# Kernel tuning notes

Measured on AMD Instinct MI355X. Metric: run time of the kernel, lower is better.

## Reference

```python
import jax, jax.numpy as jnp
import numpy as np

EMBED_DIM = 64
N_POINTS = 1_000_000


def sinusoidal_embedding(vals, embed_dim):
    # vals: [B] float -> [B, embed_dim]
    half = embed_dim // 2
    log_scale = np.log(10000.0) / (half - 1)
    freqs = jnp.exp(jnp.arange(half, dtype=jnp.float32) * (-log_scale))
    ang = vals[:, None] * freqs[None, :]
    return jnp.concatenate([jnp.sin(ang), jnp.cos(ang)], axis=1)


def embed_mlp(x, w1, b1, w2, b2):
    # Linear -> LeakyReLU(0.1) -> Linear  (embedf / embedm)
    h = jax.nn.leaky_relu(x @ w1.T + b1, negative_slope=0.1)
    return h @ w2.T + b2


def setup_inputs() -> dict:
    key = jax.random.key(0)
    ks = jax.random.split(key, 12)
    d, dh = EMBED_DIM, EMBED_DIM // 2
    s = lambda fan_in: 1.0 / np.sqrt(fan_in)
    return {
        "inputs": jax.random.normal(ks[0], (1, 6, N_POINTS), dtype=jnp.float32),
        "t": jax.random.uniform(ks[1], (1,), dtype=jnp.float32) * 1000.0,
        "mask": jax.random.randint(ks[2], (N_POINTS,), 0, 2, dtype=jnp.int32),
        "pdf": jax.random.normal(ks[3], (N_POINTS, d), dtype=jnp.float32),
        # embedf params: Linear(d,d), Linear(d,d//2)
        "ef_w1": jax.random.uniform(ks[4], (d, d), minval=-s(d), maxval=s(d)),
        "ef_b1": jnp.zeros((d,), jnp.float32),
        "ef_w2": jax.random.uniform(ks[5], (dh, d), minval=-s(d), maxval=s(d)),
        "ef_b2": jnp.zeros((dh,), jnp.float32),
        # embedm params
        "em_w1": jax.random.uniform(ks[6], (d, d), minval=-s(d), maxval=s(d)),
        "em_b1": jnp.zeros((d,), jnp.float32),
        "em_w2": jax.random.uniform(ks[7], (dh, d), minval=-s(d), maxval=s(d)),
        "em_b2": jnp.zeros((dh,), jnp.float32),
    }


def reference(inputs, t, mask, pdf, ef_w1, ef_b1, ef_w2, ef_b2, em_w1, em_b1, em_w2, em_b2):
    n = inputs.shape[-1]
    # pdf branch: [N, 64] -> [1, 64, N]
    pdf_cnl = pdf.T[None]  # [1, 64, N]
    # timestep embedding -> embedf -> broadcast over points
    te = embed_mlp(sinusoidal_embedding(t, EMBED_DIM), ef_w1, ef_b1, ef_w2, ef_b2)  # [1, 32]
    temb = jnp.broadcast_to(te[:, :, None], (te.shape[0], te.shape[1], n))  # [1, 32, N]
    # per-point mask embedding -> embedm
    me = embed_mlp(sinusoidal_embedding(mask.astype(jnp.float32), EMBED_DIM), em_w1, em_b1, em_w2, em_b2)  # [N, 32]
    memb = me.T[None]  # [1, 32, N]
    temb = jnp.concatenate([temb, memb], axis=1)  # [1, 64, N]
    # return conditioning tensors produced by the (truncated) forward prefix
    return jnp.concatenate([pdf_cnl, temb], axis=1)  # [1, 128, N]
```

## Files before the change

### kernel.cpp

```cpp
#include <hip/hip_runtime.h>
#include <math.h>


#define HALF 32

typedef float v4f __attribute__((ext_vector_type(4)));

__global__ void embed_small_kernel(const float* __restrict__ t,
                                   const float* __restrict__ ef_w1, const float* __restrict__ ef_b1,
                                   const float* __restrict__ ef_w2, const float* __restrict__ ef_b2,
                                   const float* __restrict__ em_w1, const float* __restrict__ em_b1,
                                   const float* __restrict__ em_w2, const float* __restrict__ em_b2,
                                   float* __restrict__ ws) {
    __shared__ float h[3][64];
    const int tid = threadIdx.x;
    const float log_scale = 0.2970934777f;

    if (tid < 192) {
        const int v = tid >> 6;
        const int j = tid & 63;
        const float val = (v == 0) ? t[0] : (float)(v - 1);
        const float* w1 = (v == 0) ? ef_w1 : em_w1;
        const float* b1 = (v == 0) ? ef_b1 : em_b1;
        float acc = b1[j];
        for (int k = 0; k < HALF; ++k) {
            float f = expf(-(float)k * log_scale);
            float ang = val * f;
            float s, c;
            sincosf(ang, &s, &c);
            acc += s * w1[j * 64 + k] + c * w1[j * 64 + HALF + k];
        }
        h[v][j] = (acc > 0.0f) ? acc : 0.1f * acc;
    }
    __syncthreads();
    if (tid < 96) {
        const int v = tid >> 5;
        const int c = tid & 31;
        const float* w2 = (v == 0) ? ef_w2 : em_w2;
        const float* b2 = (v == 0) ? ef_b2 : em_b2;
        float acc = b2[c];
        for (int j = 0; j < 64; ++j) acc += h[v][j] * w2[c * 64 + j];
        ws[v * 32 + c] = acc;
    }
}

__global__ __launch_bounds__(256) void pvcnn_cond_kernel(
        const float* __restrict__ pdf,
        const int* __restrict__ mask,
        const float* __restrict__ ws,
        float* __restrict__ out,
        int N) {
    __shared__ float tile[64][65];
    __shared__ float emb[96];

    const int tid = threadIdx.x;

    const int nwg  = gridDim.x;
    const int q    = nwg >> 3;
    const int r    = nwg & 7;
    const int xcd  = blockIdx.x & 7;
    const int j    = blockIdx.x >> 3;
    const int bid  = (xcd < r ? xcd * (q + 1) : r * (q + 1) + (xcd - r) * q) + j;

    const long long p0 = (long long)bid * 64;
    const bool full = (p0 + 64 <= (long long)N);

    if (tid < 96) emb[tid] = ws[tid];

    if (full) {
        const v4f* pdf4 = (const v4f*)(pdf + p0 * 64);
        #pragma unroll
        for (int it = 0; it < 4; ++it) {
            int f = tid + it * 256;
            int p = f >> 4;
            int qq = f & 15;
            v4f v = pdf4[p * 16 + qq];
            tile[p][4 * qq + 0] = v.x;
            tile[p][4 * qq + 1] = v.y;
            tile[p][4 * qq + 2] = v.z;
            tile[p][4 * qq + 3] = v.w;
        }
    } else {
        #pragma unroll
        for (int it = 0; it < 4; ++it) {
            int f = tid + it * 256;
            int p = f >> 4;
            int qq = f & 15;
            v4f v = {0.f, 0.f, 0.f, 0.f};
            if (p0 + p < (long long)N) {
                const v4f* pdf4 = (const v4f*)(pdf + (p0 + p) * 64);
                v = pdf4[qq];
            }
            tile[p][4 * qq + 0] = v.x;
            tile[p][4 * qq + 1] = v.y;
            tile[p][4 * qq + 2] = v.z;
            tile[p][4 * qq + 3] = v.w;
        }
    }

    const int p  = tid & 63;
    const int wv = tid >> 6;
    const bool pok = (p0 + p < (long long)N);
    int mval = 0;
    if (pok) mval = mask[p0 + p];

    __syncthreads();

    if (pok) {
        const long long col = p0 + p;
        #pragma unroll
        for (int cb = 0; cb < 64; cb += 4) {
            int c = cb + wv;
            __builtin_nontemporal_store(tile[p][c], out + (long long)c * N + col);
        }
        #pragma unroll
        for (int cb = 0; cb < 32; cb += 4) {
            int c = cb + wv;
            __builtin_nontemporal_store(emb[c], out + (long long)(64 + c) * N + col);
        }
        #pragma unroll
        for (int cb = 0; cb < 32; cb += 4) {
            int c = cb + wv;
            __builtin_nontemporal_store(mval ? emb[64 + c] : emb[32 + c],
                                        out + (long long)(96 + c) * N + col);
        }
    }
}

extern "C" void kernel_launch(void* const* d_in, const int* in_sizes, int n_in,
                              void* d_out, int out_size, void* d_ws, size_t ws_size,
                              hipStream_t stream) {
    const float* t     = (const float*)d_in[1];
    const int*   mask  = (const int*)d_in[2];
    const float* pdf   = (const float*)d_in[3];
    const float* ef_w1 = (const float*)d_in[4];
    const float* ef_b1 = (const float*)d_in[5];
    const float* ef_w2 = (const float*)d_in[6];
    const float* ef_b2 = (const float*)d_in[7];
    const float* em_w1 = (const float*)d_in[8];
    const float* em_b1 = (const float*)d_in[9];
    const float* em_w2 = (const float*)d_in[10];
    const float* em_b2 = (const float*)d_in[11];

    float* out = (float*)d_out;
    float* ws  = (float*)d_ws;
    const int N = in_sizes[2];

    embed_small_kernel<<<1, 192, 0, stream>>>(t, ef_w1, ef_b1, ef_w2, ef_b2,
                                              em_w1, em_b1, em_w2, em_b2, ws);

    const int nblocks = (N + 63) / 64;
    pvcnn_cond_kernel<<<nblocks, 256, 0, stream>>>(pdf, mask, ws, out, N);
}
```

Before: 136.5 us.

## Split broadcast/mask rows into separate vectorized kernel from pdf transpose

Splits the fused kernel in two. One kernel writes the 64 embedding rows with 128-bit nontemporal stores, handling 4 columns per thread and loading the mask as int4. The other kernel only does the pdf transpose. The aim is to replace scalar 32-bit stores on the broadcast half of the output with wide stores, at the cost of an extra kernel launch and the loss of overlap between the two kinds of traffic.

```diff
diff --git a/kernel.cpp b/kernel.cpp
--- a/kernel.cpp
+++ b/kernel.cpp
@@ -5,6 +5,7 @@
 #define HALF 32
 
 typedef float v4f __attribute__((ext_vector_type(4)));
+typedef int   v4i __attribute__((ext_vector_type(4)));
 
 __global__ void embed_small_kernel(const float* __restrict__ t,
                                    const float* __restrict__ ef_w1, const float* __restrict__ ef_b1,
@@ -44,28 +45,90 @@
     }
 }
 
-__global__ __launch_bounds__(256) void pvcnn_cond_kernel(
-        const float* __restrict__ pdf,
+#define BC 1024
+
+__global__ __launch_bounds__(256) void bcast_kernel(
         const int* __restrict__ mask,
         const float* __restrict__ ws,
         float* __restrict__ out,
         int N) {
+    __shared__ float emb[96];
+    const int tid = threadIdx.x;
+
+    const int nwg = gridDim.x;
+    const int q   = nwg >> 3;
+    const int r8  = nwg & 7;
+    const int xcd = blockIdx.x & 7;
+    const int j8  = blockIdx.x >> 3;
+    const int bid = (xcd < r8 ? xcd * (q + 1) : r8 * (q + 1) + (xcd - r8) * q) + j8;
+
+    const long long c0 = (long long)bid * BC;
+    const bool full = (c0 + BC <= (long long)N);
+    const long long col = c0 + 4 * tid;
+
+    if (tid < 96) emb[tid] = ws[tid];
+
+    v4i m4 = {0, 0, 0, 0};
+    if (full) {
+        m4 = ((const v4i*)mask)[(c0 >> 2) + tid];
+    } else {
+        if (col + 0 < N) m4.x = mask[col + 0];
+        if (col + 1 < N) m4.y = mask[col + 1];
+        if (col + 2 < N) m4.z = mask[col + 2];
+        if (col + 3 < N) m4.w = mask[col + 3];
+    }
+    __syncthreads();
+
+    if (full) {
+        #pragma unroll
+        for (int c = 0; c < 32; ++c) {
+            const float e = emb[c];
+            const v4f v = (v4f){e, e, e, e};
+            __builtin_nontemporal_store(v, (v4f*)(out + (long long)(64 + c) * N + col));
+        }
+        #pragma unroll
+        for (int c = 0; c < 32; ++c) {
+            const float e0 = emb[32 + c];
+            const float e1 = emb[64 + c];
+            const v4f v = (v4f){m4.x ? e1 : e0, m4.y ? e1 : e0,
+                                m4.z ? e1 : e0, m4.w ? e1 : e0};
+            __builtin_nontemporal_store(v, (v4f*)(out + (long long)(96 + c) * N + col));
+        }
+    } else {
+        for (int c = 0; c < 32; ++c) {
+            const float e = emb[c];
+            for (int d = 0; d < 4; ++d)
+                if (col + d < (long long)N)
+                    out[(long long)(64 + c) * N + col + d] = e;
+        }
+        for (int c = 0; c < 32; ++c) {
+            const float e0 = emb[32 + c];
+            const float e1 = emb[64 + c];
+            const int mm[4] = {m4.x, m4.y, m4.z, m4.w};
+            for (int d = 0; d < 4; ++d)
+                if (col + d < (long long)N)
+                    out[(long long)(96 + c) * N + col + d] = mm[d] ? e1 : e0;
+        }
+    }
+}
+
+__global__ __launch_bounds__(256) void transpose_kernel(
+        const float* __restrict__ pdf,
+        float* __restrict__ out,
+        int N) {
     __shared__ float tile[64][65];
-    __shared__ float emb[96];
 
     const int tid = threadIdx.x;
 
-    const int nwg  = gridDim.x;
-    const int q    = nwg >> 3;
-    const int r    = nwg & 7;
-    const int xcd  = blockIdx.x & 7;
-    const int j    = blockIdx.x >> 3;
-    const int bid  = (xcd < r ? xcd * (q + 1) : r * (q + 1) + (xcd - r) * q) + j;
+    const int nwg = gridDim.x;
+    const int q   = nwg >> 3;
+    const int r8  = nwg & 7;
+    const int xcd = blockIdx.x & 7;
+    const int j8  = blockIdx.x >> 3;
+    const int bid = (xcd < r8 ? xcd * (q + 1) : r8 * (q + 1) + (xcd - r8) * q) + j8;
 
     const long long p0 = (long long)bid * 64;
     const bool full = (p0 + 64 <= (long long)N);
-
-    if (tid < 96) emb[tid] = ws[tid];
 
     if (full) {
         const v4f* pdf4 = (const v4f*)(pdf + p0 * 64);
@@ -101,8 +164,6 @@
     const int p  = tid & 63;
     const int wv = tid >> 6;
     const bool pok = (p0 + p < (long long)N);
-    int mval = 0;
-    if (pok) mval = mask[p0 + p];
 
     __syncthreads();
 
@@ -112,17 +173,6 @@
         for (int cb = 0; cb < 64; cb += 4) {
             int c = cb + wv;
             __builtin_nontemporal_store(tile[p][c], out + (long long)c * N + col);
-        }
-        #pragma unroll
-        for (int cb = 0; cb < 32; cb += 4) {
-            int c = cb + wv;
-            __builtin_nontemporal_store(emb[c], out + (long long)(64 + c) * N + col);
-        }
-        #pragma unroll
-        for (int cb = 0; cb < 32; cb += 4) {
-            int c = cb + wv;
-            __builtin_nontemporal_store(mval ? emb[64 + c] : emb[32 + c],
-                                        out + (long long)(96 + c) * N + col);
         }
     }
 }
@@ -149,6 +199,9 @@
     embed_small_kernel<<<1, 192, 0, stream>>>(t, ef_w1, ef_b1, ef_w2, ef_b2,
                                               em_w1, em_b1, em_w2, em_b2, ws);
 
-    const int nblocks = (N + 63) / 64;
-    pvcnn_cond_kernel<<<nblocks, 256, 0, stream>>>(pdf, mask, ws, out, N);
-}
+    const int nb_b = (N + BC - 1) / BC;
+    bcast_kernel<<<nb_b, 256, 0, stream>>>(mask, ws, out, N);
+
+    const int nb_t = (N + 63) / 64;
+    transpose_kernel<<<nb_t, 256, 0, stream>>>(pdf, out, N);
+}
```

After: 143.8 us. +5.4%, slower.

## Widen transpose tile to 256 points per 1024-thread block with column-major LDS

Applied to the files above, without the earlier changes.

Each block now handles 256 points with 1024 threads instead of 64 points with 256 threads. The shared tile is stored channel-major with padding, so each output row write covers 256 contiguous floats (1 KB) per block instead of 256 bytes. This is meant to improve write coalescing and cut block-scheduling overhead on a memory-bound transpose. In exchange, LDS use per block grows to about 66 KB, which lowers how many blocks fit on a CU, and the transposing LDS writes may hit more bank conflicts.

```diff
diff --git a/kernel.cpp b/kernel.cpp
--- a/kernel.cpp
+++ b/kernel.cpp
@@ -3,6 +3,7 @@
 
 
 #define HALF 32
+#define PTS 256
 
 typedef float v4f __attribute__((ext_vector_type(4)));
 
@@ -44,85 +45,96 @@
     }
 }
 
-__global__ __launch_bounds__(256) void pvcnn_cond_kernel(
+__global__ __launch_bounds__(1024) void pvcnn_cond_kernel(
         const float* __restrict__ pdf,
         const int* __restrict__ mask,
         const float* __restrict__ ws,
         float* __restrict__ out,
         int N) {
-    __shared__ float tile[64][65];
+    __shared__ float tile[64 * 257];
     __shared__ float emb[96];
 
     const int tid = threadIdx.x;
 
-    const int nwg  = gridDim.x;
-    const int q    = nwg >> 3;
-    const int r    = nwg & 7;
-    const int xcd  = blockIdx.x & 7;
-    const int j    = blockIdx.x >> 3;
-    const int bid  = (xcd < r ? xcd * (q + 1) : r * (q + 1) + (xcd - r) * q) + j;
+    const int nwg = gridDim.x;
+    const int q   = nwg >> 3;
+    const int r8  = nwg & 7;
+    const int xcd = blockIdx.x & 7;
+    const int j8  = blockIdx.x >> 3;
+    const int bid = (xcd < r8 ? xcd * (q + 1) : r8 * (q + 1) + (xcd - r8) * q) + j8;
 
-    const long long p0 = (long long)bid * 64;
-    const bool full = (p0 + 64 <= (long long)N);
+    const long long p0 = (long long)bid * PTS;
+    const bool full = (p0 + PTS <= (long long)N);
 
     if (tid < 96) emb[tid] = ws[tid];
 
     if (full) {
-        const v4f* pdf4 = (const v4f*)(pdf + p0 * 64);
+        const v4f* src = (const v4f*)(pdf + p0 * 64);
         #pragma unroll
         for (int it = 0; it < 4; ++it) {
-            int f = tid + it * 256;
-            int p = f >> 4;
-            int qq = f & 15;
-            v4f v = pdf4[p * 16 + qq];
-            tile[p][4 * qq + 0] = v.x;
-            tile[p][4 * qq + 1] = v.y;
-            tile[p][4 * qq + 2] = v.z;
-            tile[p][4 * qq + 3] = v.w;
+            const int f = tid + it * 1024;
+            const int p = f >> 4;
+            const int qq = f & 15;
+            const v4f v = src[f];
+            const int b = (4 * qq) * 257 + p;
+            tile[b + 0 * 257] = v.x;
+            tile[b + 1 * 257] = v.y;
+            tile[b + 2 * 257] = v.z;
+            tile[b + 3 * 257] = v.w;
         }
     } else {
         #pragma unroll
         for (int it = 0; it < 4; ++it) {
-            int f = tid + it * 256;
-            int p = f >> 4;
-            int qq = f & 15;
+            const int f = tid + it * 1024;
+            const int p = f >> 4;
+            const int qq = f & 15;
             v4f v = {0.f, 0.f, 0.f, 0.f};
-            if (p0 + p < (long long)N) {
-                const v4f* pdf4 = (const v4f*)(pdf + (p0 + p) * 64);
-                v = pdf4[qq];
-            }
-            tile[p][4 * qq + 0] = v.x;
-            tile[p][4 * qq + 1] = v.y;
-            tile[p][4 * qq + 2] = v.z;
-            tile[p][4 * qq + 3] = v.w;
+            if (p0 + p < (long long)N)
+                v = ((const v4f*)(pdf + (p0 + p) * 64))[qq];
+            const int b = (4 * qq) * 257 + p;
+            tile[b + 0 * 257] = v.x;
+            tile[b + 1 * 257] = v.y;
+            tile[b + 2 * 257] = v.z;
+            tile[b + 3 * 257] = v.w;
         }
     }
 
-    const int p  = tid & 63;
-    const int wv = tid >> 6;
-    const bool pok = (p0 + p < (long long)N);
+    const int c  = tid & 255;
+    const int rg = tid >> 8;
+    const long long col = p0 + c;
+    const bool cok = (col < (long long)N);
+
     int mval = 0;
-    if (pok) mval = mask[p0 + p];
+    if (cok) mval = mask[col];
 
     __syncthreads();
 
-    if (pok) {
-        const long long col = p0 + p;
+    if (full) {
         #pragma unroll
-        for (int cb = 0; cb < 64; cb += 4) {
-            int c = cb + wv;
-            __builtin_nontemporal_store(tile[p][c], out + (long long)c * N + col);
+        for (int rr = 0; rr < 32; ++rr) {
+            const int r = rg + 4 * rr;
+            float v;
+            if (rr < 16) {
+                v = tile[r * 257 + c];
+            } else if (rr < 24) {
+                v = emb[r - 64];
+            } else {
+                v = mval ? emb[64 + (r - 96)] : emb[32 + (r - 96)];
+            }
+            __builtin_nontemporal_store(v, out + (long long)r * N + col);
         }
-        #pragma unroll
-        for (int cb = 0; cb < 32; cb += 4) {
-            int c = cb + wv;
-            __builtin_nontemporal_store(emb[c], out + (long long)(64 + c) * N + col);
-        }
-        #pragma unroll
-        for (int cb = 0; cb < 32; cb += 4) {
-            int c = cb + wv;
-            __builtin_nontemporal_store(mval ? emb[64 + c] : emb[32 + c],
-                                        out + (long long)(96 + c) * N + col);
+    } else if (cok) {
+        for (int rr = 0; rr < 32; ++rr) {
+            const int r = rg + 4 * rr;
+            float v;
+            if (rr < 16) {
+                v = tile[r * 257 + c];
+            } else if (rr < 24) {
+                v = emb[r - 64];
+            } else {
+                v = mval ? emb[64 + (r - 96)] : emb[32 + (r - 96)];
+            }
+            __builtin_nontemporal_store(v, out + (long long)r * N + col);
         }
     }
 }
@@ -149,6 +161,6 @@
     embed_small_kernel<<<1, 192, 0, stream>>>(t, ef_w1, ef_b1, ef_w2, ef_b2,
                                               em_w1, em_b1, em_w2, em_b2, ws);
 
-    const int nblocks = (N + 63) / 64;
-    pvcnn_cond_kernel<<<nblocks, 256, 0, stream>>>(pdf, mask, ws, out, N);
+    const int nblocks = (N + PTS - 1) / PTS;
+    pvcnn_cond_kernel<<<nblocks, 1024, 0, stream>>>(pdf, mask, ws, out, N);
 }
```

New measurement: 130.6 us (median of 2 runs). 1.05x faster.
